# Kernel optimization log

Hardware: AMD Instinct MI355X
Metric: run time of the kernel (lower is better)

Reference implementation:

```python
import jax, jax.numpy as jnp
import numpy as np

N_NODES = 50000
NEG_SLOPE = 0.01  # default leaky_relu slope in torch/F.leaky_relu


def sage_gcn_layer(x, src, dst, W, b):
    # DGL SAGEConv with aggregator_type='gcn':
    #   h_neigh[v] = (sum_{(u->v) in E} x[u] + x[v]) / (in_deg(v) + 1)
    #   out = h_neigh @ W + b
    msg = jax.ops.segment_sum(x[src], dst, num_segments=N_NODES)  # [N, d]
    deg = jax.ops.segment_sum(jnp.ones_like(dst, dtype=x.dtype), dst,
                              num_segments=N_NODES)               # [N]
    h = (msg + x) / (deg + 1.0)[:, None]
    return h @ W + b


def setup_inputs() -> dict:
    key = jax.random.key(0)
    ks = jax.random.split(key, 5)
    in_feats, h_feats, num_classes = 128, 128, 32
    n_edges = 800000
    in_feat = jax.random.normal(ks[0], (N_NODES, in_feats), dtype=jnp.float32)
    edges = jax.random.randint(ks[1], (2, n_edges), 0, N_NODES, dtype=jnp.int64)
    W1 = jax.random.normal(ks[2], (in_feats, h_feats), dtype=jnp.float32) / np.sqrt(in_feats)
    b1 = jnp.zeros((h_feats,), dtype=jnp.float32)
    W2 = jax.random.normal(ks[3], (h_feats, num_classes), dtype=jnp.float32) / np.sqrt(h_feats)
    b2 = jnp.zeros((num_classes,), dtype=jnp.float32)
    return {"in_feat": in_feat, "edges": edges, "W1": W1, "b1": b1, "W2": W2, "b2": b2}


def reference(in_feat, edges, W1, b1, W2, b2):
    src, dst = edges[0], edges[1]
    h = sage_gcn_layer(in_feat, src, dst, W1, b1)      # conv1
    h = jnp.where(h >= 0, h, NEG_SLOPE * h)            # leaky_relu
    h = sage_gcn_layer(h, src, dst, W2, b2)            # conv2
    return h
```

## Files before the change

### kernel.cpp

```cpp
#include <hip/hip_runtime.h>

#define N_NODES  50000
#define F_IN     128
#define F_H      128
#define F_OUT    32
#define N_EDGES  800000
#define NEG_SLOPE 0.01f
#define NBUCKET   196
#define EDGE_BLOCKS 784
#define EPB       1024
#define GEMM1_BLOCKS 782
#define GEMM2_BLOCKS 391

typedef short bf16x8 __attribute__((ext_vector_type(8)));
typedef float f32x4  __attribute__((ext_vector_type(4)));

__device__ __forceinline__ float bf2f(unsigned short h) {
    return __uint_as_float(((unsigned)h) << 16);
}
__device__ __forceinline__ unsigned short f2bf(float f) {
    unsigned u = __float_as_uint(f);
    u += 0x7FFF + ((u >> 16) & 1);
    return (unsigned short)(u >> 16);
}

__global__ __launch_bounds__(256) void prep_kernel(
    const float* __restrict__ W1, const float* __restrict__ W2,
    unsigned short* __restrict__ W1b, unsigned short* __restrict__ W2b)
{
    int idx = (blockIdx.x * 256 + threadIdx.x) * 4;
    if (idx < 16384) {
        float4 v = *(const float4*)(W1 + idx);
        ushort4 o;
        o.x = f2bf(v.x); o.y = f2bf(v.y); o.z = f2bf(v.z); o.w = f2bf(v.w);
        *(ushort4*)(W1b + idx) = o;
    } else {
        int j = idx - 16384;
        if (j < 4096) {
            float4 v = *(const float4*)(W2 + j);
            ushort4 o;
            o.x = f2bf(v.x); o.y = f2bf(v.y); o.z = f2bf(v.z); o.w = f2bf(v.w);
            *(ushort4*)(W2b + j) = o;
        }
    }
}

__global__ __launch_bounds__(256) void hist_gemm1_kernel(
    const int* __restrict__ dst, int* __restrict__ counts,
    const float* __restrict__ x, const unsigned short* __restrict__ W1b,
    unsigned short* __restrict__ yb)
{
    __shared__ alignas(16) unsigned short Xl[64 * 136];
    int b = blockIdx.x;
    int t = threadIdx.x;

    if (b < EDGE_BLOCKS) {
        int* hist = (int*)Xl;
        for (int i = t; i < NBUCKET; i += 256) hist[i] = 0;
        __syncthreads();
        int base = b * EPB;
        for (int r = 0; r < EPB / 256; ++r) {
            int e = base + r * 256 + t;
            if (e < N_EDGES) atomicAdd(&hist[dst[e] >> 8], 1);
        }
        __syncthreads();
        for (int i = t; i < NBUCKET; i += 256)
            counts[i * EDGE_BLOCKS + b] = hist[i];
        return;
    }

    int g  = b - EDGE_BLOCKS;
    int vb = g * 64;

    for (int i4 = t; i4 < 2048; i4 += 256) {
        int flat = i4 * 4;
        int r = flat >> 7;
        int k = flat & 127;
        int v = vb + r;
        float4 xv = (v < N_NODES) ? *(const float4*)(x + (size_t)v * 128 + k)
                                  : make_float4(0.f, 0.f, 0.f, 0.f);
        ushort4 o;
        o.x = f2bf(xv.x); o.y = f2bf(xv.y); o.z = f2bf(xv.z); o.w = f2bf(xv.w);
        *(ushort4*)(Xl + r * 136 + k) = o;
    }

    int wv   = t >> 6;
    int lane = t & 63;
    int quad = lane >> 4;
    int lc   = lane & 15;
    int c0   = wv * 32;

    bf16x8 bfr[2][4];
    for (int ct = 0; ct < 2; ++ct)
        for (int ks = 0; ks < 4; ++ks) {
            bf16x8 tmp;
            #pragma unroll
            for (int j = 0; j < 8; ++j)
                tmp[j] = (short)W1b[(ks * 32 + quad * 8 + j) * 128 + c0 + ct * 16 + lc];
            bfr[ct][ks] = tmp;
        }

    __syncthreads();

    f32x4 acc[4][2];
    for (int rt = 0; rt < 4; ++rt)
        for (int ct = 0; ct < 2; ++ct)
            acc[rt][ct] = (f32x4){0.f, 0.f, 0.f, 0.f};

    for (int rt = 0; rt < 4; ++rt) {
        int row = rt * 16 + lc;
        #pragma unroll
        for (int ks = 0; ks < 4; ++ks) {
            bf16x8 af = *(const bf16x8*)(Xl + row * 136 + ks * 32 + quad * 8);
            acc[rt][0] = __builtin_amdgcn_mfma_f32_16x16x32_bf16(af, bfr[0][ks], acc[rt][0], 0, 0, 0);
            acc[rt][1] = __builtin_amdgcn_mfma_f32_16x16x32_bf16(af, bfr[1][ks], acc[rt][1], 0, 0, 0);
        }
    }

    for (int rt = 0; rt < 4; ++rt)
        for (int ct = 0; ct < 2; ++ct)
            #pragma unroll
            for (int r = 0; r < 4; ++r) {
                int grow = vb + rt * 16 + quad * 4 + r;
                if (grow < N_NODES)
                    yb[(size_t)grow * 128 + c0 + ct * 16 + lc] = f2bf(acc[rt][ct][r]);
            }
}

__global__ __launch_bounds__(256) void scan_cols_kernel(
    int* __restrict__ counts, int* __restrict__ bucket_total)
{
    __shared__ int c[256];
    int t = threadIdx.x;
    int carry = 0;
    for (int ch = 0; ch < (EDGE_BLOCKS + 255) / 256; ++ch) {
        int ci = ch * 256 + t;
        int cv = (ci < EDGE_BLOCKS) ? counts[blockIdx.x * EDGE_BLOCKS + ci] : 0;
        c[t] = cv;
        __syncthreads();
        for (int off = 1; off < 256; off <<= 1) {
            int a = c[t];
            int add = (t >= off) ? c[t - off] : 0;
            __syncthreads();
            c[t] = a + add;
            __syncthreads();
        }
        if (ci < EDGE_BLOCKS)
            counts[blockIdx.x * EDGE_BLOCKS + ci] = carry + c[t] - cv;
        carry += c[255];
        __syncthreads();
    }
    if (t == 0) bucket_total[blockIdx.x] = carry;
}

__global__ __launch_bounds__(256) void bucket_base_kernel(
    const int* __restrict__ bucket_total, int* __restrict__ bucket_base)
{
    __shared__ int s[256];
    int t = threadIdx.x;
    int v = (t < NBUCKET) ? bucket_total[t] : 0;
    s[t] = v;
    __syncthreads();
    for (int off = 1; off < 256; off <<= 1) {
        int a = s[t];
        int add = (t >= off) ? s[t - off] : 0;
        __syncthreads();
        s[t] = a + add;
        __syncthreads();
    }
    if (t < NBUCKET) bucket_base[t] = s[t] - v;
    if (t == 0) bucket_base[NBUCKET] = s[NBUCKET - 1];
}

__global__ __launch_bounds__(256) void bin_kernel(
    const int* __restrict__ src, const int* __restrict__ dst,
    const int* __restrict__ rel, const int* __restrict__ bucket_base,
    unsigned int* __restrict__ bins)
{
    __shared__ int pos[NBUCKET];
    int blk = blockIdx.x;
    int t = threadIdx.x;
    for (int i = t; i < NBUCKET; i += 256)
        pos[i] = bucket_base[i] + rel[i * EDGE_BLOCKS + blk];
    __syncthreads();
    int base = blk * EPB;
    for (int r = 0; r < EPB / 256; ++r) {
        int e = base + r * 256 + t;
        if (e < N_EDGES) {
            int d = dst[e];
            int sy = src[e];
            int p = atomicAdd(&pos[d >> 8], 1);
            bins[p] = ((unsigned)d << 16) | (unsigned)sy;
        }
    }
}

__global__ __launch_bounds__(256) void bucket_sort_kernel(
    const unsigned int* __restrict__ bins, const int* __restrict__ bucket_base,
    int* __restrict__ row_ptr, int* __restrict__ csr)
{
    __shared__ int cnt[256];
    __shared__ int cur[256];
    int b = blockIdx.x;
    int t = threadIdx.x;
    int nlo = b * 256;
    int beg = bucket_base[b];
    int end = bucket_base[b + 1];
    cnt[t] = 0;
    __syncthreads();
    for (int i = beg + t; i < end; i += 256)
        atomicAdd(&cnt[(bins[i] >> 16) & 255], 1);
    __syncthreads();
    int v = cnt[t];
    cur[t] = v;
    __syncthreads();
    for (int off = 1; off < 256; off <<= 1) {
        int a = cur[t];
        int add = (t >= off) ? cur[t - off] : 0;
        __syncthreads();
        cur[t] = a + add;
        __syncthreads();
    }
    int start = beg + cur[t] - v;
    int node = nlo + t;
    if (node < N_NODES) row_ptr[node] = start;
    cur[t] = start;
    if (b == 0 && t == 0) row_ptr[N_NODES] = N_EDGES;
    __syncthreads();
    for (int i = beg + t; i < end; i += 256) {
        unsigned w = bins[i];
        int dl = (w >> 16) & 255;
        int p = atomicAdd(&cur[dl], 1);
        csr[p] = (int)(w & 0xFFFFu);
    }
}

__global__ __launch_bounds__(256) void aggregate128_kernel(
    const unsigned short* __restrict__ yb, const int* __restrict__ row_ptr,
    const int* __restrict__ csr, const float* __restrict__ b1,
    unsigned short* __restrict__ h1b)
{
    int gw = (blockIdx.x * 256 + threadIdx.x) >> 5;
    int l4 = (threadIdx.x & 31) * 4;
    if (gw >= N_NODES) return;
    int beg = row_ptr[gw];
    int end = row_ptr[gw + 1];
    ushort4 us = *(const ushort4*)(yb + (size_t)gw * 128 + l4);
    float ax = bf2f(us.x), ay = bf2f(us.y), az = bf2f(us.z), aw = bf2f(us.w);
    float bx = 0.f, by = 0.f, bz = 0.f, bw = 0.f;
    int p = beg;
    for (; p + 3 < end; p += 4) {
        int s0 = csr[p], s1 = csr[p + 1], s2 = csr[p + 2], s3 = csr[p + 3];
        ushort4 u0 = *(const ushort4*)(yb + (size_t)s0 * 128 + l4);
        ushort4 u1 = *(const ushort4*)(yb + (size_t)s1 * 128 + l4);
        ushort4 u2 = *(const ushort4*)(yb + (size_t)s2 * 128 + l4);
        ushort4 u3 = *(const ushort4*)(yb + (size_t)s3 * 128 + l4);
        ax += bf2f(u0.x) + bf2f(u2.x); ay += bf2f(u0.y) + bf2f(u2.y);
        az += bf2f(u0.z) + bf2f(u2.z); aw += bf2f(u0.w) + bf2f(u2.w);
        bx += bf2f(u1.x) + bf2f(u3.x); by += bf2f(u1.y) + bf2f(u3.y);
        bz += bf2f(u1.z) + bf2f(u3.z); bw += bf2f(u1.w) + bf2f(u3.w);
    }
    for (; p < end; ++p) {
        int s0 = csr[p];
        ushort4 u0 = *(const ushort4*)(yb + (size_t)s0 * 128 + l4);
        ax += bf2f(u0.x); ay += bf2f(u0.y); az += bf2f(u0.z); aw += bf2f(u0.w);
    }
    float rec = 1.0f / (float)(end - beg + 1);
    float4 bb = *(const float4*)(b1 + l4);
    float vx = (ax + bx) * rec + bb.x;
    float vy = (ay + by) * rec + bb.y;
    float vz = (az + bz) * rec + bb.z;
    float vw = (aw + bw) * rec + bb.w;
    vx = (vx >= 0.f) ? vx : NEG_SLOPE * vx;
    vy = (vy >= 0.f) ? vy : NEG_SLOPE * vy;
    vz = (vz >= 0.f) ? vz : NEG_SLOPE * vz;
    vw = (vw >= 0.f) ? vw : NEG_SLOPE * vw;
    ushort4 o;
    o.x = f2bf(vx); o.y = f2bf(vy); o.z = f2bf(vz); o.w = f2bf(vw);
    *(ushort4*)(h1b + (size_t)gw * 128 + l4) = o;
}

__global__ __launch_bounds__(256) void aggregate32_kernel(
    const unsigned short* __restrict__ zb, const int* __restrict__ row_ptr,
    const int* __restrict__ csr, const float* __restrict__ b2,
    float* __restrict__ out)
{
    int g  = (blockIdx.x * 256 + threadIdx.x) >> 3;
    int l4 = (threadIdx.x & 7) * 4;
    if (g >= N_NODES) return;
    int beg = row_ptr[g];
    int end = row_ptr[g + 1];
    ushort4 us = *(const ushort4*)(zb + (size_t)g * 32 + l4);
    float ax = bf2f(us.x), ay = bf2f(us.y), az = bf2f(us.z), aw = bf2f(us.w);
    float bx = 0.f, by = 0.f, bz = 0.f, bw = 0.f;
    int p = beg;
    for (; p + 3 < end; p += 4) {
        int s0 = csr[p], s1 = csr[p + 1], s2 = csr[p + 2], s3 = csr[p + 3];
        ushort4 u0 = *(const ushort4*)(zb + (size_t)s0 * 32 + l4);
        ushort4 u1 = *(const ushort4*)(zb + (size_t)s1 * 32 + l4);
        ushort4 u2 = *(const ushort4*)(zb + (size_t)s2 * 32 + l4);
        ushort4 u3 = *(const ushort4*)(zb + (size_t)s3 * 32 + l4);
        ax += bf2f(u0.x) + bf2f(u2.x); ay += bf2f(u0.y) + bf2f(u2.y);
        az += bf2f(u0.z) + bf2f(u2.z); aw += bf2f(u0.w) + bf2f(u2.w);
        bx += bf2f(u1.x) + bf2f(u3.x); by += bf2f(u1.y) + bf2f(u3.y);
        bz += bf2f(u1.z) + bf2f(u3.z); bw += bf2f(u1.w) + bf2f(u3.w);
    }
    for (; p < end; ++p) {
        int s0 = csr[p];
        ushort4 u0 = *(const ushort4*)(zb + (size_t)s0 * 32 + l4);
        ax += bf2f(u0.x); ay += bf2f(u0.y); az += bf2f(u0.z); aw += bf2f(u0.w);
    }
    float rec = 1.0f / (float)(end - beg + 1);
    float4 bb = *(const float4*)(b2 + l4);
    float4 o;
    o.x = (ax + bx) * rec + bb.x;
    o.y = (ay + by) * rec + bb.y;
    o.z = (az + bz) * rec + bb.z;
    o.w = (aw + bw) * rec + bb.w;
    *(float4*)(out + (size_t)g * 32 + l4) = o;
}

__global__ __launch_bounds__(256) void gemm2z_kernel(
    const unsigned short* __restrict__ h1b,
    const unsigned short* __restrict__ W2b, unsigned short* __restrict__ zb)
{
    int t    = threadIdx.x;
    int wv   = t >> 6;
    int lane = t & 63;
    int quad = lane >> 4;
    int lc   = lane & 15;

    bf16x8 bfr[2][4];
    for (int ct = 0; ct < 2; ++ct)
        for (int ks = 0; ks < 4; ++ks) {
            bf16x8 tmp;
            #pragma unroll
            for (int j = 0; j < 8; ++j)
                tmp[j] = (short)W2b[(ks * 32 + quad * 8 + j) * 32 + ct * 16 + lc];
            bfr[ct][ks] = tmp;
        }

    f32x4 acc[2][2];
    for (int rt = 0; rt < 2; ++rt)
        for (int ct = 0; ct < 2; ++ct)
            acc[rt][ct] = (f32x4){0.f, 0.f, 0.f, 0.f};

    int vb = blockIdx.x * 128 + wv * 32;
    for (int rt = 0; rt < 2; ++rt) {
        int row = vb + rt * 16 + lc;
        int vrow = (row < N_NODES) ? row : 0;
        #pragma unroll
        for (int ks = 0; ks < 4; ++ks) {
            bf16x8 af = *(const bf16x8*)(h1b + (size_t)vrow * 128 + ks * 32 + quad * 8);
            acc[rt][0] = __builtin_amdgcn_mfma_f32_16x16x32_bf16(af, bfr[0][ks], acc[rt][0], 0, 0, 0);
            acc[rt][1] = __builtin_amdgcn_mfma_f32_16x16x32_bf16(af, bfr[1][ks], acc[rt][1], 0, 0, 0);
        }
    }

    for (int rt = 0; rt < 2; ++rt)
        for (int ct = 0; ct < 2; ++ct)
            #pragma unroll
            for (int r = 0; r < 4; ++r) {
                int grow = vb + rt * 16 + quad * 4 + r;
                if (grow < N_NODES)
                    zb[(size_t)grow * 32 + ct * 16 + lc] = f2bf(acc[rt][ct][r]);
            }
}

__global__ __launch_bounds__(256) void scatter_kernel(
    const float* __restrict__ x, const int* __restrict__ src,
    const int* __restrict__ dst, float* __restrict__ msg,
    float* __restrict__ deg, int nE)
{
    int tid  = blockIdx.x * 256 + threadIdx.x;
    int e    = tid >> 5;
    int lane = tid & 31;
    if (e >= nE) return;
    int s = src[e];
    int d = dst[e];
    if (deg != nullptr && lane == 0) atomicAdd(&deg[d], 1.0f);
    float4 v = *(const float4*)(x + (size_t)s * F_IN + lane * 4);
    float* mp = msg + (size_t)d * F_IN + lane * 4;
    atomicAdd(mp + 0, v.x);
    atomicAdd(mp + 1, v.y);
    atomicAdd(mp + 2, v.z);
    atomicAdd(mp + 3, v.w);
}

__global__ __launch_bounds__(256) void normalize_kernel(
    const float* __restrict__ self, const float* __restrict__ deg,
    float* __restrict__ msg)
{
    int idx = blockIdx.x * 256 + threadIdx.x;
    int v = idx >> 5;
    int c = (idx & 31) * 4;
    if (v >= N_NODES) return;
    float rec = 1.0f / (deg[v] + 1.0f);
    float4 m = *(const float4*)(msg  + (size_t)v * 128 + c);
    float4 s = *(const float4*)(self + (size_t)v * 128 + c);
    m.x = (m.x + s.x) * rec;
    m.y = (m.y + s.y) * rec;
    m.z = (m.z + s.z) * rec;
    m.w = (m.w + s.w) * rec;
    *(float4*)(msg + (size_t)v * 128 + c) = m;
}

__global__ __launch_bounds__(256) void gemm1_kernel(
    const float* __restrict__ msg, const float* __restrict__ W,
    const float* __restrict__ b, float* __restrict__ h)
{
    __shared__ float Wl[128 * 68];
    __shared__ float Rl[32 * 132];
    int t     = threadIdx.x;
    int vb    = blockIdx.x * 32;
    int jbase = blockIdx.y * 64;
    for (int i4 = t; i4 < 2048; i4 += 256) {
        int flat = i4 * 4;
        int k  = flat >> 6;
        int jj = flat & 63;
        *(float4*)(Wl + k * 68 + jj) = *(const float4*)(W + k * F_H + jbase + jj);
    }
    for (int i4 = t; i4 < 1024; i4 += 256) {
        int flat = i4 * 4;
        int r = flat >> 7;
        int k = flat & 127;
        int v = vb + r;
        float4 sv = (v < N_NODES) ? *(const float4*)(msg + (size_t)v * F_IN + k)
                                  : make_float4(0.f, 0.f, 0.f, 0.f);
        *(float4*)(Rl + r * 132 + k) = sv;
    }
    __syncthreads();
    int j0 = (t & 15) * 4;
    int r0 = (t >> 4) * 2;
    float acc[2][4] = {{0.f,0.f,0.f,0.f},{0.f,0.f,0.f,0.f}};
    for (int k = 0; k < 128; ++k) {
        float4 w = *(const float4*)(Wl + k * 68 + j0);
        float s0 = Rl[(r0    ) * 132 + k];
        float s1 = Rl[(r0 + 1) * 132 + k];
        acc[0][0] += s0 * w.x; acc[0][1] += s0 * w.y;
        acc[0][2] += s0 * w.z; acc[0][3] += s0 * w.w;
        acc[1][0] += s1 * w.x; acc[1][1] += s1 * w.y;
        acc[1][2] += s1 * w.z; acc[1][3] += s1 * w.w;
    }
    for (int i = 0; i < 2; ++i) {
        int v = vb + r0 + i;
        if (v >= N_NODES) continue;
        float4 o;
        o.x = acc[i][0] + b[jbase + j0 + 0];
        o.y = acc[i][1] + b[jbase + j0 + 1];
        o.z = acc[i][2] + b[jbase + j0 + 2];
        o.w = acc[i][3] + b[jbase + j0 + 3];
        o.x = (o.x >= 0.f) ? o.x : NEG_SLOPE * o.x;
        o.y = (o.y >= 0.f) ? o.y : NEG_SLOPE * o.y;
        o.z = (o.z >= 0.f) ? o.z : NEG_SLOPE * o.z;
        o.w = (o.w >= 0.f) ? o.w : NEG_SLOPE * o.w;
        *(float4*)(h + (size_t)v * F_H + jbase + j0) = o;
    }
}

__global__ __launch_bounds__(256) void gemm2_kernel(
    const float* __restrict__ msg, const float* __restrict__ W,
    const float* __restrict__ b, float* __restrict__ out)
{
    __shared__ float Wl[128 * 36];
    __shared__ float Rl[64 * 132];
    int t  = threadIdx.x;
    int vb = blockIdx.x * 64;
    for (int i4 = t; i4 < 1024; i4 += 256) {
        int flat = i4 * 4;
        int k  = flat >> 5;
        int jj = flat & 31;
        *(float4*)(Wl + k * 36 + jj) = *(const float4*)(W + k * F_OUT + jj);
    }
    for (int i4 = t; i4 < 2048; i4 += 256) {
        int flat = i4 * 4;
        int r = flat >> 7;
        int k = flat & 127;
        int v = vb + r;
        float4 sv = (v < N_NODES) ? *(const float4*)(msg + (size_t)v * F_H + k)
                                  : make_float4(0.f, 0.f, 0.f, 0.f);
        *(float4*)(Rl + r * 132 + k) = sv;
    }
    __syncthreads();
    int j0 = (t & 7) * 4;
    int r0 = (t >> 3) * 2;
    float acc[2][4] = {{0.f,0.f,0.f,0.f},{0.f,0.f,0.f,0.f}};
    for (int k = 0; k < 128; ++k) {
        float4 w = *(const float4*)(Wl + k * 36 + j0);
        float s0 = Rl[(r0    ) * 132 + k];
        float s1 = Rl[(r0 + 1) * 132 + k];
        acc[0][0] += s0 * w.x; acc[0][1] += s0 * w.y;
        acc[0][2] += s0 * w.z; acc[0][3] += s0 * w.w;
        acc[1][0] += s1 * w.x; acc[1][1] += s1 * w.y;
        acc[1][2] += s1 * w.z; acc[1][3] += s1 * w.w;
    }
    for (int i = 0; i < 2; ++i) {
        int v = vb + r0 + i;
        if (v >= N_NODES) continue;
        float4 o;
        o.x = acc[i][0] + b[j0 + 0];
        o.y = acc[i][1] + b[j0 + 1];
        o.z = acc[i][2] + b[j0 + 2];
        o.w = acc[i][3] + b[j0 + 3];
        *(float4*)(out + (size_t)v * F_OUT + j0) = o;
    }
}

extern "C" void kernel_launch(void* const* d_in, const int* in_sizes, int n_in,
                              void* d_out, int out_size, void* d_ws, size_t ws_size,
                              hipStream_t stream)
{
    const float* x     = (const float*)d_in[0];
    const int*   edges = (const int*)d_in[1];
    const float* W1    = (const float*)d_in[2];
    const float* b1    = (const float*)d_in[3];
    const float* W2    = (const float*)d_in[4];
    const float* b2    = (const float*)d_in[5];
    float* out = (float*)d_out;

    const int* src = edges;
    const int* dst = edges + N_EDGES;

    const size_t INT_WORDS = 256ull + 256ull + 50432ull + 800000ull
                           + 153664ull + 800000ull;
    const size_t SHORTS = 6400000ull + 6400000ull + 1600000ull + 16384ull + 4096ull;
    const size_t FAST_BYTES = INT_WORDS * 4 + SHORTS * 2;

    if (ws_size >= FAST_BYTES) {
        int*   bucket_total = (int*)d_ws;
        int*   bucket_base  = bucket_total + 256;
        int*   row_ptr      = bucket_base + 256;
        int*   csr          = row_ptr + 50432;
        int*   counts       = csr + 800000;
        unsigned int* bins  = (unsigned int*)(counts + 153664);
        unsigned short* yb  = (unsigned short*)(bins + 800000);
        unsigned short* h1b = yb + 6400000;
        unsigned short* zb  = h1b + 6400000;
        unsigned short* W1b = zb + 1600000;
        unsigned short* W2b = W1b + 16384;

        prep_kernel<<<20, 256, 0, stream>>>(W1, W2, W1b, W2b);
        hist_gemm1_kernel<<<EDGE_BLOCKS + GEMM1_BLOCKS, 256, 0, stream>>>(
            dst, counts, x, W1b, yb);
        scan_cols_kernel<<<NBUCKET, 256, 0, stream>>>(counts, bucket_total);
        bucket_base_kernel<<<1, 256, 0, stream>>>(bucket_total, bucket_base);
        bin_kernel<<<EDGE_BLOCKS, 256, 0, stream>>>(src, dst, counts,
                                                    bucket_base, bins);
        bucket_sort_kernel<<<NBUCKET, 256, 0, stream>>>(bins, bucket_base,
                                                        row_ptr, csr);
        int ab1 = (N_NODES * 32 + 255) / 256;
        aggregate128_kernel<<<ab1, 256, 0, stream>>>(yb, row_ptr, csr, b1, h1b);
        gemm2z_kernel<<<GEMM2_BLOCKS, 256, 0, stream>>>(h1b, W2b, zb);
        int ab2 = (N_NODES * 8 + 255) / 256;
        aggregate32_kernel<<<ab2, 256, 0, stream>>>(zb, row_ptr, csr, b2, out);
    } else {
        float* deg = (float*)d_ws;
        float* msg = deg + 50176;
        float* h1  = msg + (size_t)N_NODES * F_H;

        hipMemsetAsync(d_ws, 0, (50176 + (size_t)N_NODES * F_H) * sizeof(float), stream);
        int sb = (N_EDGES * 32 + 255) / 256;
        int nb = (N_NODES * 32 + 255) / 256;

        scatter_kernel<<<sb, 256, 0, stream>>>(x, src, dst, msg, deg, N_EDGES);
        normalize_kernel<<<nb, 256, 0, stream>>>(x, deg, msg);
        gemm1_kernel<<<dim3((N_NODES + 31) / 32, 2), 256, 0, stream>>>(msg, W1, b1, h1);

        hipMemsetAsync(msg, 0, (size_t)N_NODES * F_H * sizeof(float), stream);
        scatter_kernel<<<sb, 256, 0, stream>>>(h1, src, dst, msg, nullptr, N_EDGES);
        normalize_kernel<<<nb, 256, 0, stream>>>(h1, deg, msg);
        gemm2_kernel<<<(N_NODES + 63) / 64, 256, 0, stream>>>(msg, W2, b2, out);
    }
}
```

Baseline: 168.9 us.

## Drop prep and bucket-base kernels, widen aggregation loads to 16 bytes

Removes the weight-conversion prep kernel and instead converts W1/W2 to bf16 inline when each GEMM block loads its B fragments. The single-block bucket-base scan is removed; bin_kernel and bucket_sort_kernel each redo the 196-entry prefix scan locally. Both aggregation kernels now have each lane load 8 bf16 values (uint4) with half as many lanes per node and a 2-way unroll instead of 4-way. This cuts two launches and the serial dependency they add, at the cost of redundant per-block scans and conversions, and of less memory-level parallelism per node in the gathers.

```diff
diff --git a/kernel.cpp b/kernel.cpp
--- a/kernel.cpp
+++ b/kernel.cpp
@@ -23,31 +23,12 @@
     u += 0x7FFF + ((u >> 16) & 1);
     return (unsigned short)(u >> 16);
 }
-
-__global__ __launch_bounds__(256) void prep_kernel(
-    const float* __restrict__ W1, const float* __restrict__ W2,
-    unsigned short* __restrict__ W1b, unsigned short* __restrict__ W2b)
-{
-    int idx = (blockIdx.x * 256 + threadIdx.x) * 4;
-    if (idx < 16384) {
-        float4 v = *(const float4*)(W1 + idx);
-        ushort4 o;
-        o.x = f2bf(v.x); o.y = f2bf(v.y); o.z = f2bf(v.z); o.w = f2bf(v.w);
-        *(ushort4*)(W1b + idx) = o;
-    } else {
-        int j = idx - 16384;
-        if (j < 4096) {
-            float4 v = *(const float4*)(W2 + j);
-            ushort4 o;
-            o.x = f2bf(v.x); o.y = f2bf(v.y); o.z = f2bf(v.z); o.w = f2bf(v.w);
-            *(ushort4*)(W2b + j) = o;
-        }
-    }
-}
+__device__ __forceinline__ float bflo(unsigned u) { return __uint_as_float(u << 16); }
+__device__ __forceinline__ float bfhi(unsigned u) { return __uint_as_float(u & 0xFFFF0000u); }
 
 __global__ __launch_bounds__(256) void hist_gemm1_kernel(
     const int* __restrict__ dst, int* __restrict__ counts,
-    const float* __restrict__ x, const unsigned short* __restrict__ W1b,
+    const float* __restrict__ x, const float* __restrict__ W1,
     unsigned short* __restrict__ yb)
 {
     __shared__ alignas(16) unsigned short Xl[64 * 136];
@@ -96,7 +77,7 @@
             bf16x8 tmp;
             #pragma unroll
             for (int j = 0; j < 8; ++j)
-                tmp[j] = (short)W1b[(ks * 32 + quad * 8 + j) * 128 + c0 + ct * 16 + lc];
+                tmp[j] = (short)f2bf(W1[(ks * 32 + quad * 8 + j) * 128 + c0 + ct * 16 + lc]);
             bfr[ct][ks] = tmp;
         }
 
@@ -127,6 +108,7 @@
             }
 }
 
+
 __global__ __launch_bounds__(256) void scan_cols_kernel(
     int* __restrict__ counts, int* __restrict__ bucket_total)
 {
@@ -153,13 +135,17 @@
     if (t == 0) bucket_total[blockIdx.x] = carry;
 }
 
-__global__ __launch_bounds__(256) void bucket_base_kernel(
-    const int* __restrict__ bucket_total, int* __restrict__ bucket_base)
+__global__ __launch_bounds__(256) void bin_kernel(
+    const int* __restrict__ src, const int* __restrict__ dst,
+    const int* __restrict__ rel, const int* __restrict__ bucket_total,
+    unsigned int* __restrict__ bins)
 {
     __shared__ int s[256];
+    __shared__ int pos[NBUCKET];
+    int blk = blockIdx.x;
     int t = threadIdx.x;
-    int v = (t < NBUCKET) ? bucket_total[t] : 0;
-    s[t] = v;
+    int bt = (t < NBUCKET) ? bucket_total[t] : 0;
+    s[t] = bt;
     __syncthreads();
     for (int off = 1; off < 256; off <<= 1) {
         int a = s[t];
@@ -168,20 +154,8 @@
         s[t] = a + add;
         __syncthreads();
     }
-    if (t < NBUCKET) bucket_base[t] = s[t] - v;
-    if (t == 0) bucket_base[NBUCKET] = s[NBUCKET - 1];
-}
-
-__global__ __launch_bounds__(256) void bin_kernel(
-    const int* __restrict__ src, const int* __restrict__ dst,
-    const int* __restrict__ rel, const int* __restrict__ bucket_base,
-    unsigned int* __restrict__ bins)
-{
-    __shared__ int pos[NBUCKET];
-    int blk = blockIdx.x;
-    int t = threadIdx.x;
-    for (int i = t; i < NBUCKET; i += 256)
-        pos[i] = bucket_base[i] + rel[i * EDGE_BLOCKS + blk];
+    if (t < NBUCKET)
+        pos[t] = (s[t] - bt) + rel[t * EDGE_BLOCKS + blk];
     __syncthreads();
     int base = blk * EPB;
     for (int r = 0; r < EPB / 256; ++r) {
@@ -196,16 +170,26 @@
 }
 
 __global__ __launch_bounds__(256) void bucket_sort_kernel(
-    const unsigned int* __restrict__ bins, const int* __restrict__ bucket_base,
+    const unsigned int* __restrict__ bins, const int* __restrict__ bucket_total,
     int* __restrict__ row_ptr, int* __restrict__ csr)
 {
+    __shared__ int s[256];
     __shared__ int cnt[256];
     __shared__ int cur[256];
     int b = blockIdx.x;
     int t = threadIdx.x;
-    int nlo = b * 256;
-    int beg = bucket_base[b];
-    int end = bucket_base[b + 1];
+    int bt = (t < NBUCKET) ? bucket_total[t] : 0;
+    s[t] = bt;
+    __syncthreads();
+    for (int off = 1; off < 256; off <<= 1) {
+        int a = s[t];
+        int add = (t >= off) ? s[t - off] : 0;
+        __syncthreads();
+        s[t] = a + add;
+        __syncthreads();
+    }
+    int beg = (b == 0) ? 0 : s[b - 1];
+    int end = s[b];
     cnt[t] = 0;
     __syncthreads();
     for (int i = beg + t; i < end; i += 256)
@@ -222,7 +206,7 @@
         __syncthreads();
     }
     int start = beg + cur[t] - v;
-    int node = nlo + t;
+    int node = b * 256 + t;
     if (node < N_NODES) row_ptr[node] = start;
     cur[t] = start;
     if (b == 0 && t == 0) row_ptr[N_NODES] = N_EDGES;
@@ -235,49 +219,63 @@
     }
 }
 
+
 __global__ __launch_bounds__(256) void aggregate128_kernel(
     const unsigned short* __restrict__ yb, const int* __restrict__ row_ptr,
     const int* __restrict__ csr, const float* __restrict__ b1,
     unsigned short* __restrict__ h1b)
 {
-    int gw = (blockIdx.x * 256 + threadIdx.x) >> 5;
-    int l4 = (threadIdx.x & 31) * 4;
+    int gw = (blockIdx.x * 256 + threadIdx.x) >> 4;
+    int l8 = (threadIdx.x & 15) * 8;
     if (gw >= N_NODES) return;
     int beg = row_ptr[gw];
     int end = row_ptr[gw + 1];
-    ushort4 us = *(const ushort4*)(yb + (size_t)gw * 128 + l4);
-    float ax = bf2f(us.x), ay = bf2f(us.y), az = bf2f(us.z), aw = bf2f(us.w);
-    float bx = 0.f, by = 0.f, bz = 0.f, bw = 0.f;
+    uint4 us = *(const uint4*)(yb + (size_t)gw * 128 + l8);
+    float a0 = bflo(us.x), a1 = bfhi(us.x), a2 = bflo(us.y), a3 = bfhi(us.y);
+    float a4 = bflo(us.z), a5 = bfhi(us.z), a6 = bflo(us.w), a7 = bfhi(us.w);
+    float c0 = 0.f, c1 = 0.f, c2 = 0.f, c3 = 0.f;
+    float c4 = 0.f, c5 = 0.f, c6 = 0.f, c7 = 0.f;
     int p = beg;
-    for (; p + 3 < end; p += 4) {
-        int s0 = csr[p], s1 = csr[p + 1], s2 = csr[p + 2], s3 = csr[p + 3];
-        ushort4 u0 = *(const ushort4*)(yb + (size_t)s0 * 128 + l4);
-        ushort4 u1 = *(const ushort4*)(yb + (size_t)s1 * 128 + l4);
-        ushort4 u2 = *(const ushort4*)(yb + (size_t)s2 * 128 + l4);
-        ushort4 u3 = *(const ushort4*)(yb + (size_t)s3 * 128 + l4);
-        ax += bf2f(u0.x) + bf2f(u2.x); ay += bf2f(u0.y) + bf2f(u2.y);
-        az += bf2f(u0.z) + bf2f(u2.z); aw += bf2f(u0.w) + bf2f(u2.w);
-        bx += bf2f(u1.x) + bf2f(u3.x); by += bf2f(u1.y) + bf2f(u3.y);
-        bz += bf2f(u1.z) + bf2f(u3.z); bw += bf2f(u1.w) + bf2f(u3.w);
-    }
-    for (; p < end; ++p) {
+    for (; p + 1 < end; p += 2) {
+        int s0 = csr[p], s1 = csr[p + 1];
+        uint4 u0 = *(const uint4*)(yb + (size_t)s0 * 128 + l8);
+        uint4 u1 = *(const uint4*)(yb + (size_t)s1 * 128 + l8);
+        a0 += bflo(u0.x); a1 += bfhi(u0.x); a2 += bflo(u0.y); a3 += bfhi(u0.y);
+        a4 += bflo(u0.z); a5 += bfhi(u0.z); a6 += bflo(u0.w); a7 += bfhi(u0.w);
+        c0 += bflo(u1.x); c1 += bfhi(u1.x); c2 += bflo(u1.y); c3 += bfhi(u1.y);
+        c4 += bflo(u1.z); c5 += bfhi(u1.z); c6 += bflo(u1.w); c7 += bfhi(u1.w);
+    }
+    if (p < end) {
         int s0 = csr[p];
-        ushort4 u0 = *(const ushort4*)(yb + (size_t)s0 * 128 + l4);
-        ax += bf2f(u0.x); ay += bf2f(u0.y); az += bf2f(u0.z); aw += bf2f(u0.w);
+        uint4 u0 = *(const uint4*)(yb + (size_t)s0 * 128 + l8);
+        a0 += bflo(u0.x); a1 += bfhi(u0.x); a2 += bflo(u0.y); a3 += bfhi(u0.y);
+        a4 += bflo(u0.z); a5 += bfhi(u0.z); a6 += bflo(u0.w); a7 += bfhi(u0.w);
     }
     float rec = 1.0f / (float)(end - beg + 1);
-    float4 bb = *(const float4*)(b1 + l4);
-    float vx = (ax + bx) * rec + bb.x;
-    float vy = (ay + by) * rec + bb.y;
-    float vz = (az + bz) * rec + bb.z;
-    float vw = (aw + bw) * rec + bb.w;
-    vx = (vx >= 0.f) ? vx : NEG_SLOPE * vx;
-    vy = (vy >= 0.f) ? vy : NEG_SLOPE * vy;
-    vz = (vz >= 0.f) ? vz : NEG_SLOPE * vz;
-    vw = (vw >= 0.f) ? vw : NEG_SLOPE * vw;
-    ushort4 o;
-    o.x = f2bf(vx); o.y = f2bf(vy); o.z = f2bf(vz); o.w = f2bf(vw);
-    *(ushort4*)(h1b + (size_t)gw * 128 + l4) = o;
+    float4 bb0 = *(const float4*)(b1 + l8);
+    float4 bb1 = *(const float4*)(b1 + l8 + 4);
+    float v0 = (a0 + c0) * rec + bb0.x;
+    float v1 = (a1 + c1) * rec + bb0.y;
+    float v2 = (a2 + c2) * rec + bb0.z;
+    float v3 = (a3 + c3) * rec + bb0.w;
+    float v4 = (a4 + c4) * rec + bb1.x;
+    float v5 = (a5 + c5) * rec + bb1.y;
+    float v6 = (a6 + c6) * rec + bb1.z;
+    float v7 = (a7 + c7) * rec + bb1.w;
+    v0 = (v0 >= 0.f) ? v0 : NEG_SLOPE * v0;
+    v1 = (v1 >= 0.f) ? v1 : NEG_SLOPE * v1;
+    v2 = (v2 >= 0.f) ? v2 : NEG_SLOPE * v2;
+    v3 = (v3 >= 0.f) ? v3 : NEG_SLOPE * v3;
+    v4 = (v4 >= 0.f) ? v4 : NEG_SLOPE * v4;
+    v5 = (v5 >= 0.f) ? v5 : NEG_SLOPE * v5;
+    v6 = (v6 >= 0.f) ? v6 : NEG_SLOPE * v6;
+    v7 = (v7 >= 0.f) ? v7 : NEG_SLOPE * v7;
+    uint4 o;
+    o.x = (unsigned)f2bf(v0) | ((unsigned)f2bf(v1) << 16);
+    o.y = (unsigned)f2bf(v2) | ((unsigned)f2bf(v3) << 16);
+    o.z = (unsigned)f2bf(v4) | ((unsigned)f2bf(v5) << 16);
+    o.w = (unsigned)f2bf(v6) | ((unsigned)f2bf(v7) << 16);
+    *(uint4*)(h1b + (size_t)gw * 128 + l8) = o;
 }
 
 __global__ __launch_bounds__(256) void aggregate32_kernel(
@@ -285,44 +283,51 @@
     const int* __restrict__ csr, const float* __restrict__ b2,
     float* __restrict__ out)
 {
-    int g  = (blockIdx.x * 256 + threadIdx.x) >> 3;
-    int l4 = (threadIdx.x & 7) * 4;
+    int g  = (blockIdx.x * 256 + threadIdx.x) >> 2;
+    int l8 = (threadIdx.x & 3) * 8;
     if (g >= N_NODES) return;
     int beg = row_ptr[g];
     int end = row_ptr[g + 1];
-    ushort4 us = *(const ushort4*)(zb + (size_t)g * 32 + l4);
-    float ax = bf2f(us.x), ay = bf2f(us.y), az = bf2f(us.z), aw = bf2f(us.w);
-    float bx = 0.f, by = 0.f, bz = 0.f, bw = 0.f;
+    uint4 us = *(const uint4*)(zb + (size_t)g * 32 + l8);
+    float a0 = bflo(us.x), a1 = bfhi(us.x), a2 = bflo(us.y), a3 = bfhi(us.y);
+    float a4 = bflo(us.z), a5 = bfhi(us.z), a6 = bflo(us.w), a7 = bfhi(us.w);
+    float c0 = 0.f, c1 = 0.f, c2 = 0.f, c3 = 0.f;
+    float c4 = 0.f, c5 = 0.f, c6 = 0.f, c7 = 0.f;
     int p = beg;
-    for (; p + 3 < end; p += 4) {
-        int s0 = csr[p], s1 = csr[p + 1], s2 = csr[p + 2], s3 = csr[p + 3];
-        ushort4 u0 = *(const ushort4*)(zb + (size_t)s0 * 32 + l4);
-        ushort4 u1 = *(const ushort4*)(zb + (size_t)s1 * 32 + l4);
-        ushort4 u2 = *(const ushort4*)(zb + (size_t)s2 * 32 + l4);
-        ushort4 u3 = *(const ushort4*)(zb + (size_t)s3 * 32 + l4);
-        ax += bf2f(u0.x) + bf2f(u2.x); ay += bf2f(u0.y) + bf2f(u2.y);
-        az += bf2f(u0.z) + bf2f(u2.z); aw += bf2f(u0.w) + bf2f(u2.w);
-        bx += bf2f(u1.x) + bf2f(u3.x); by += bf2f(u1.y) + bf2f(u3.y);
-        bz += bf2f(u1.z) + bf2f(u3.z); bw += bf2f(u1.w) + bf2f(u3.w);
-    }
-    for (; p < end; ++p) {
+    for (; p + 1 < end; p += 2) {
+        int s0 = csr[p], s1 = csr[p + 1];
+        uint4 u0 = *(const uint4*)(zb + (size_t)s0 * 32 + l8);
+        uint4 u1 = *(const uint4*)(zb + (size_t)s1 * 32 + l8);
+        a0 += bflo(u0.x); a1 += bfhi(u0.x); a2 += bflo(u0.y); a3 += bfhi(u0.y);
+        a4 += bflo(u0.z); a5 += bfhi(u0.z); a6 += bflo(u0.w); a7 += bfhi(u0.w);
+        c0 += bflo(u1.x); c1 += bfhi(u1.x); c2 += bflo(u1.y); c3 += bfhi(u1.y);
+        c4 += bflo(u1.z); c5 += bfhi(u1.z); c6 += bflo(u1.w); c7 += bfhi(u1.w);
+    }
+    if (p < end) {
         int s0 = csr[p];
-        ushort4 u0 = *(const ushort4*)(zb + (size_t)s0 * 32 + l4);
-        ax += bf2f(u0.x); ay += bf2f(u0.y); az += bf2f(u0.z); aw += bf2f(u0.w);
+        uint4 u0 = *(const uint4*)(zb + (size_t)s0 * 32 + l8);
+        a0 += bflo(u0.x); a1 += bfhi(u0.x); a2 += bflo(u0.y); a3 += bfhi(u0.y);
+        a4 += bflo(u0.z); a5 += bfhi(u0.z); a6 += bflo(u0.w); a7 += bfhi(u0.w);
     }
     float rec = 1.0f / (float)(end - beg + 1);
-    float4 bb = *(const float4*)(b2 + l4);
-    float4 o;
-    o.x = (ax + bx) * rec + bb.x;
-    o.y = (ay + by) * rec + bb.y;
-    o.z = (az + bz) * rec + bb.z;
-    o.w = (aw + bw) * rec + bb.w;
-    *(float4*)(out + (size_t)g * 32 + l4) = o;
+    float4 bb0 = *(const float4*)(b2 + l8);
+    float4 bb1 = *(const float4*)(b2 + l8 + 4);
+    float4 o0, o1;
+    o0.x = (a0 + c0) * rec + bb0.x;
+    o0.y = (a1 + c1) * rec + bb0.y;
+    o0.z = (a2 + c2) * rec + bb0.z;
+    o0.w = (a3 + c3) * rec + bb0.w;
+    o1.x = (a4 + c4) * rec + bb1.x;
+    o1.y = (a5 + c5) * rec + bb1.y;
+    o1.z = (a6 + c6) * rec + bb1.z;
+    o1.w = (a7 + c7) * rec + bb1.w;
+    *(float4*)(out + (size_t)g * 32 + l8) = o0;
+    *(float4*)(out + (size_t)g * 32 + l8 + 4) = o1;
 }
 
 __global__ __launch_bounds__(256) void gemm2z_kernel(
     const unsigned short* __restrict__ h1b,
-    const unsigned short* __restrict__ W2b, unsigned short* __restrict__ zb)
+    const float* __restrict__ W2, unsigned short* __restrict__ zb)
 {
     int t    = threadIdx.x;
     int wv   = t >> 6;
@@ -336,7 +341,7 @@
             bf16x8 tmp;
             #pragma unroll
             for (int j = 0; j < 8; ++j)
-                tmp[j] = (short)W2b[(ks * 32 + quad * 8 + j) * 32 + ct * 16 + lc];
+                tmp[j] = (short)f2bf(W2[(ks * 32 + quad * 8 + j) * 32 + ct * 16 + lc]);
             bfr[ct][ks] = tmp;
         }
 
@@ -521,38 +526,32 @@
     const int* src = edges;
     const int* dst = edges + N_EDGES;
 
-    const size_t INT_WORDS = 256ull + 256ull + 50432ull + 800000ull
-                           + 153664ull + 800000ull;
-    const size_t SHORTS = 6400000ull + 6400000ull + 1600000ull + 16384ull + 4096ull;
+    const size_t INT_WORDS = 256ull + 50432ull + 800000ull + 153664ull + 800000ull;
+    const size_t SHORTS = 6400000ull + 6400000ull + 1600000ull;
     const size_t FAST_BYTES = INT_WORDS * 4 + SHORTS * 2;
 
     if (ws_size >= FAST_BYTES) {
         int*   bucket_total = (int*)d_ws;
-        int*   bucket_base  = bucket_total + 256;
-        int*   row_ptr      = bucket_base + 256;
+        int*   row_ptr      = bucket_total + 256;
         int*   csr          = row_ptr + 50432;
         int*   counts       = csr + 800000;
         unsigned int* bins  = (unsigned int*)(counts + 153664);
         unsigned short* yb  = (unsigned short*)(bins + 800000);
         unsigned short* h1b = yb + 6400000;
         unsigned short* zb  = h1b + 6400000;
-        unsigned short* W1b = zb + 1600000;
-        unsigned short* W2b = W1b + 16384;
-
-        prep_kernel<<<20, 256, 0, stream>>>(W1, W2, W1b, W2b);
+
         hist_gemm1_kernel<<<EDGE_BLOCKS + GEMM1_BLOCKS, 256, 0, stream>>>(
-            dst, counts, x, W1b, yb);
+            dst, counts, x, W1, yb);
         scan_cols_kernel<<<NBUCKET, 256, 0, stream>>>(counts, bucket_total);
-        bucket_base_kernel<<<1, 256, 0, stream>>>(bucket_total, bucket_base);
         bin_kernel<<<EDGE_BLOCKS, 256, 0, stream>>>(src, dst, counts,
-                                                    bucket_base, bins);
-        bucket_sort_kernel<<<NBUCKET, 256, 0, stream>>>(bins, bucket_base,
+                                                    bucket_total, bins);
+        bucket_sort_kernel<<<NBUCKET, 256, 0, stream>>>(bins, bucket_total,
                                                         row_ptr, csr);
-        int ab1 = (N_NODES * 32 + 255) / 256;
-        aggregate128_kernel<<<ab1, 256, 0, stream>>>(yb, row_ptr, csr, b1, h1b);
-        gemm2z_kernel<<<GEMM2_BLOCKS, 256, 0, stream>>>(h1b, W2b, zb);
-        int ab2 = (N_NODES * 8 + 255) / 256;
-        aggregate32_kernel<<<ab2, 256, 0, stream>>>(zb, row_ptr, csr, b2, out);
+        aggregate128_kernel<<<(N_NODES * 16 + 255) / 256, 256, 0, stream>>>(
+            yb, row_ptr, csr, b1, h1b);
+        gemm2z_kernel<<<GEMM2_BLOCKS, 256, 0, stream>>>(h1b, W2, zb);
+        aggregate32_kernel<<<(N_NODES * 4 + 255) / 256, 256, 0, stream>>>(
+            zb, row_ptr, csr, b2, out);
     } else {
         float* deg = (float*)d_ws;
         float* msg = deg + 50176;
```

Result: faster. 165.3 us (-2.2%).
